# Optimization experiments

Measured on AMD Instinct MI355X. Metric: run time of the kernel, lower is better.

The kernel has to match this reference:

```python
import jax, jax.numpy as jnp
import numpy as np

K = 6
STRIDE = 2

def _conv1d(x, w, b):
    # x: [B,1,L], w: [1,1,K] (OIW), b: [1]
    y = jax.lax.conv_general_dilated(
        x, w, window_strides=(STRIDE,), padding='VALID',
        dimension_numbers=('NCW', 'OIW', 'NCW'))
    return y + b[None, :, None]

def setup_inputs() -> dict:
    key = jax.random.key(0)
    kx, k1, k2, k3, kb1, kb2, kb3 = jax.random.split(key, 7)
    bound = 1.0 / np.sqrt(1 * K)  # torch Conv1d default init bound
    x = jax.random.normal(kx, (4096, 1, 16384), dtype=jnp.float32)
    w1 = jax.random.uniform(k1, (1, 1, K), jnp.float32, -bound, bound)
    w2 = jax.random.uniform(k2, (1, 1, K), jnp.float32, -bound, bound)
    w3 = jax.random.uniform(k3, (1, 1, K), jnp.float32, -bound, bound)
    b1 = jax.random.uniform(kb1, (1,), jnp.float32, -bound, bound)
    b2 = jax.random.uniform(kb2, (1,), jnp.float32, -bound, bound)
    b3 = jax.random.uniform(kb3, (1,), jnp.float32, -bound, bound)
    return {"x": x, "w1": w1, "b1": b1, "w2": w2, "b2": b2, "w3": w3, "b3": b3}

def reference(x, w1, b1, w2, b2, w3, b3):
    # three stacked strided valid convs, matching torch Encoder.forward
    x = _conv1d(x, w1, b1)  # [B,1,8190]
    x = _conv1d(x, w2, b2)  # [B,1,4093]
    x = _conv1d(x, w3, b3)  # [B,1,2044]
    return x
```

## Files before the change

kernel.cpp:

```cpp
#include <hip/hip_runtime.h>
#include <hip/hip_bf16.h>


#define L_IN  16384
#define L3    2044
#define KW    6
#define GROUPS (L3 / 4)

__global__ __launch_bounds__(64) void encoder_weights_kernel(
    const float* __restrict__ w1, const float* __restrict__ b1,
    const float* __restrict__ w2, const float* __restrict__ b2,
    const float* __restrict__ w3, const float* __restrict__ b3,
    float* __restrict__ wb)
{
    const int tx = threadIdx.x;
    if (tx < 36) {
        float s = 0.f;
        for (int a = 0; a < KW; ++a) {
            const int rem = tx - 4 * a;
            for (int b = 0; b < KW; ++b) {
                const int c = rem - 2 * b;
                if (c >= 0 && c < KW) s += w3[a] * w2[b] * w1[c];
            }
        }
        wb[tx] = s;
    } else if (tx == 36) {
        float s3 = 0.f, s2 = 0.f;
        for (int i = 0; i < KW; ++i) { s3 += w3[i]; s2 += w2[i]; }
        wb[36] = b3[0] + b2[0] * s3 + b1[0] * s2 * s3;
    }
}

__device__ __forceinline__ float uniform_load(const float* p) {
    return __uint_as_float(__builtin_amdgcn_readfirstlane(__float_as_uint(*p)));
}

__global__ __launch_bounds__(256) void encoder_main_kernel(
    const float* __restrict__ x,
    const float* __restrict__ wb,
    float* __restrict__ out)
{
    const int t = blockIdx.x * blockDim.x + threadIdx.x;
    const int row = blockIdx.y;
    if (t >= GROUPS) return;
    const int j3 = 4 * t;

    float W[36];
#pragma unroll
    for (int k = 0; k < 36; ++k) W[k] = uniform_load(wb + k);
    const float Beff = uniform_load(wb + 36);

    const float* xr = x + (size_t)row * L_IN + 8 * (size_t)j3;
    const float4* xv = reinterpret_cast<const float4*>(xr);
    float v[60];
#pragma unroll
    for (int i = 0; i < 15; ++i) {
        float4 q = xv[i];
        v[4 * i + 0] = q.x;
        v[4 * i + 1] = q.y;
        v[4 * i + 2] = q.z;
        v[4 * i + 3] = q.w;
    }

    float acc[4];
#pragma unroll
    for (int i = 0; i < 4; ++i) {
        float s = Beff;
#pragma unroll
        for (int k = 0; k < 36; ++k) s = fmaf(W[k], v[8 * i + k], s);
        acc[i] = s;
    }

    float4 o;
    o.x = acc[0]; o.y = acc[1]; o.z = acc[2]; o.w = acc[3];
    *reinterpret_cast<float4*>(out + (size_t)row * L3 + j3) = o;
}

extern "C" void kernel_launch(void* const* d_in, const int* in_sizes, int n_in,
                              void* d_out, int out_size, void* d_ws, size_t ws_size,
                              hipStream_t stream) {
    const float* x  = (const float*)d_in[0];
    const float* w1 = (const float*)d_in[1];
    const float* b1 = (const float*)d_in[2];
    const float* w2 = (const float*)d_in[3];
    const float* b2 = (const float*)d_in[4];
    const float* w3 = (const float*)d_in[5];
    const float* b3 = (const float*)d_in[6];
    float* out = (float*)d_out;
    float* wb  = (float*)d_ws;

    const int B = in_sizes[0] / L_IN;

    encoder_weights_kernel<<<1, 64, 0, stream>>>(w1, b1, w2, b2, w3, b3, wb);

    dim3 block(256);
    dim3 grid((GROUPS + 255) / 256, B);
    encoder_main_kernel<<<grid, block, 0, stream>>>(x, wb, out);
}
```

Measured before the change: 396.4 us.

## Stage each input row in padded LDS and compute eight outputs per thread

Each block now handles one full input row. It loads the row into shared memory with coalesced float4 reads, using a padded layout to avoid bank conflicts. Each thread then slides a register window over LDS to produce eight outputs. This replaces the earlier overlapping per-thread global loads, which fetched about twice the unique data. The cost is a large LDS footprint that limits each CU to about two blocks, which lowers occupancy and latency hiding, and adds a block-wide barrier.

```diff
diff --git a/kernel.cpp b/kernel.cpp
--- a/kernel.cpp
+++ b/kernel.cpp
@@ -5,7 +5,10 @@
 #define L_IN  16384
 #define L3    2044
 #define KW    6
-#define GROUPS (L3 / 4)
+
+__device__ __forceinline__ int pad_slot(int g) { return g + 4 * (g >> 6); }
+
+#define LDS_FLOATS 17440
 
 __global__ __launch_bounds__(64) void encoder_weights_kernel(
     const float* __restrict__ w1, const float* __restrict__ b1,
@@ -35,45 +38,62 @@
     return __uint_as_float(__builtin_amdgcn_readfirstlane(__float_as_uint(*p)));
 }
 
-__global__ __launch_bounds__(256) void encoder_main_kernel(
+__global__ __launch_bounds__(256, 2) void encoder_main_kernel(
     const float* __restrict__ x,
     const float* __restrict__ wb,
     float* __restrict__ out)
 {
-    const int t = blockIdx.x * blockDim.x + threadIdx.x;
-    const int row = blockIdx.y;
-    if (t >= GROUPS) return;
-    const int j3 = 4 * t;
+    __shared__ float s[LDS_FLOATS];
+
+    const int t   = threadIdx.x;
+    const int row = blockIdx.x;
+
+    const float* xr = x + (size_t)row * L_IN;
+#pragma unroll
+    for (int i = 0; i < 16; ++i) {
+        const int f = 4 * (t + 256 * i);
+        float4 q = *reinterpret_cast<const float4*>(xr + f);
+        *reinterpret_cast<float4*>(&s[pad_slot(f)]) = q;
+    }
 
     float W[36];
 #pragma unroll
     for (int k = 0; k < 36; ++k) W[k] = uniform_load(wb + k);
     const float Beff = uniform_load(wb + 36);
 
-    const float* xr = x + (size_t)row * L_IN + 8 * (size_t)j3;
-    const float4* xv = reinterpret_cast<const float4*>(xr);
-    float v[60];
+    __syncthreads();
+
+    const int g0 = 64 * t;
+    float v[36];
 #pragma unroll
-    for (int i = 0; i < 15; ++i) {
-        float4 q = xv[i];
-        v[4 * i + 0] = q.x;
-        v[4 * i + 1] = q.y;
-        v[4 * i + 2] = q.z;
-        v[4 * i + 3] = q.w;
+    for (int j = 0; j < 9; ++j)
+        *reinterpret_cast<float4*>(&v[4 * j]) =
+            *reinterpret_cast<const float4*>(&s[pad_slot(g0 + 4 * j)]);
+
+    float r[8];
+#pragma unroll
+    for (int i = 0; i < 8; ++i) {
+        if (i > 0) {
+#pragma unroll
+            for (int k = 0; k < 28; ++k) v[k] = v[k + 8];
+            *reinterpret_cast<float4*>(&v[28]) =
+                *reinterpret_cast<const float4*>(&s[pad_slot(g0 + 8 * i + 28)]);
+            *reinterpret_cast<float4*>(&v[32]) =
+                *reinterpret_cast<const float4*>(&s[pad_slot(g0 + 8 * i + 32)]);
+        }
+        float acc = Beff;
+#pragma unroll
+        for (int k = 0; k < 36; ++k) acc = fmaf(W[k], v[k], acc);
+        r[i] = acc;
     }
 
-    float acc[4];
-#pragma unroll
-    for (int i = 0; i < 4; ++i) {
-        float s = Beff;
-#pragma unroll
-        for (int k = 0; k < 36; ++k) s = fmaf(W[k], v[8 * i + k], s);
-        acc[i] = s;
+    float* orow = out + (size_t)row * L3 + 8 * t;
+    float4 o0; o0.x = r[0]; o0.y = r[1]; o0.z = r[2]; o0.w = r[3];
+    *reinterpret_cast<float4*>(orow) = o0;
+    if (8 * t + 4 < L3) {
+        float4 o1; o1.x = r[4]; o1.y = r[5]; o1.z = r[6]; o1.w = r[7];
+        *reinterpret_cast<float4*>(orow + 4) = o1;
     }
-
-    float4 o;
-    o.x = acc[0]; o.y = acc[1]; o.z = acc[2]; o.w = acc[3];
-    *reinterpret_cast<float4*>(out + (size_t)row * L3 + j3) = o;
 }
 
 extern "C" void kernel_launch(void* const* d_in, const int* in_sizes, int n_in,
@@ -92,8 +112,5 @@
     const int B = in_sizes[0] / L_IN;
 
     encoder_weights_kernel<<<1, 64, 0, stream>>>(w1, b1, w2, b2, w3, b3, wb);
-
-    dim3 block(256);
-    dim3 grid((GROUPS + 255) / 256, B);
-    encoder_main_kernel<<<grid, block, 0, stream>>>(x, wb, out);
+    encoder_main_kernel<<<B, 256, 0, stream>>>(x, wb, out);
 }
```

After: 380.3 us. 4.1% less time.
